# Optimization experiments

Measured on AMD Instinct MI355X. Metric: run time of the kernel, lower is better.

The kernel has to match this reference:

```python
import jax, jax.numpy as jnp
import numpy as np

# Dims: T=64 steps, B=8 batch, H=128 hidden, NH=4 heads, D=2*H=256 cell dim
T, B, H, NH = 64, 8, 128, 4
D = 2 * H
EPS = 1e-5


def _bn(v, scale, bias):
    # flax BatchNorm (training mode): stats over all axes except feature (-1)
    axes = tuple(range(v.ndim - 1))
    mu = v.mean(axes, keepdims=True)
    var = v.var(axes, keepdims=True)
    return (v - mu) * jax.lax.rsqrt(var + EPS) * scale + bias


def setup_inputs() -> dict:
    key = jax.random.key(0)
    ks = iter(jax.random.split(key, 48))
    r = lambda shape, s=0.02: (jax.random.normal(next(ks), shape, jnp.float32) * s)
    z = lambda shape: jnp.zeros(shape, jnp.float32)
    o = lambda shape: jnp.ones(shape, jnp.float32)
    inp = {
        "x": jax.random.normal(next(ks), (T, B, H), jnp.float32),
        # per-head mLSTMCell params (stacked over NH heads), flax Linear: y = x @ W + b
        "Wq": r((NH, D, D)), "bq": z((NH, D)),
        "Wk": r((NH, D, D)), "bk": z((NH, D)),
        "Wv": r((NH, D, D)), "bv": z((NH, D)),
        "conv_k": r((4, 1, NH), 0.2), "conv_b": z((NH,)),  # 1->NH channel conv == per-head 1->1 conv
        "Wi": r((NH, D)), "bi": r((NH,), 0.01),
        "Wf": r((NH, D)),
        "bf": jax.random.uniform(next(ks), (NH,), jnp.float32, 3.0, 6.0),
        "Wo": r((NH, D, D)), "bo": z((NH, D)),
        "Wskip": r((NH, D, D)), "bskip": z((NH, D)),
        # block params
        "bn1_s": o((H,)), "bn1_b": z((H,)),
        "bn2_s": o((D,)), "bn2_b": z((D,)),
        "Wup1": r((H, D)), "bup1": z((D,)),
        "Wup2": r((H, D)), "bup2": z((D,)),
        "Wpoll": r((NH * D, D)), "bpoll": z((D,)),
        "Wdown": r((D, H)), "bdown": z((H,)),
    }
    return inp


def reference(x, Wq, bq, Wk, bk, Wv, bv, conv_k, conv_b, Wi, bi, Wf, bf,
              Wo, bo, Wskip, bskip, bn1_s, bn1_b, bn2_s, bn2_b,
              Wup1, bup1, Wup2, bup2, Wpoll, bpoll, Wdown, bdown):
    nh, d, _ = Wq.shape
    b = x.shape[1]
    inv_sqrt_d = 1.0 / jnp.sqrt(jnp.float32(d))

    def step(carry, xt):
        c, n, m = carry  # c: [nh,b,d,d], n: [nh,b,d], m: [nh,b]
        u = _bn(xt, bn1_s, bn1_b)                      # [b,H]
        trig = jax.nn.silu(u @ Wup2 + bup2)            # [b,d]
        xin = u @ Wup1 + bup1                          # [b,d] mlstm input
        outg = jax.nn.sigmoid(jnp.einsum('bd,hde->hbe', xin, Wo) + bo[:, None, :])
        it = jnp.einsum('bd,hd->hb', xin, Wi) + bi[:, None]
        ft = jnp.einsum('bd,hd->hb', xin, Wf) + bf[:, None]
        m_new = jnp.maximum(ft + m, it)
        ig = jnp.exp(it - m_new)
        fg = jnp.exp(ft + m - m_new)
        # causal-ish depthwise conv over feature axis (flax Conv SAME, k=4)
        qk = jax.lax.conv_general_dilated(xin[..., None], conv_k, (1,), 'SAME',
                                          dimension_numbers=('NWC', 'WIO', 'NWC')) + conv_b
        qk = jax.nn.silu(jnp.transpose(qk, (2, 0, 1)))  # [nh,b,d]
        k = (jnp.einsum('hbd,hde->hbe', qk, Wk) + bk[:, None, :]) * inv_sqrt_d
        q = jnp.einsum('hbd,hde->hbe', qk, Wq) + bq[:, None, :]
        v = jnp.einsum('bd,hde->hbe', xin, Wv) + bv[:, None, :]
        c_new = fg[:, :, None, None] * c + jnp.einsum('hb,hbi,hbj->hbij', ig, v, k)
        n_new = fg[..., None] * n + ig[..., None] * k
        scaler = 1.0 / jnp.maximum(jnp.abs(jnp.einsum('hbi,hbi->hb', n_new, q)), 1.0)
        h = outg * jnp.einsum('hbik,hbk->hbi', c_new, q) * scaler[..., None]
        h = h + jnp.einsum('hbd,hde->hbe', qk, Wskip) + bskip[:, None, :]
        ho = _bn(h, bn2_s, bn2_b)                      # [nh,b,d]
        ho = jnp.transpose(ho, (1, 0, 2)).reshape(b, nh * d)
        ho = ho @ Wpoll + bpoll                        # [b,d]
        y = (ho * trig) @ Wdown + bdown + xt           # residual
        return (c_new, n_new, m_new), y

    c0 = jnp.zeros((nh, b, d, d), x.dtype)
    n0 = jnp.zeros((nh, b, d), x.dtype)
    m0 = jnp.zeros((nh, b), x.dtype)
    _, ys = jax.lax.scan(step, (c0, n0, m0), x)
    return ys
```

## Files before the change

kernel.cpp:

```cpp
#include <hip/hip_runtime.h>
#include <hip/hip_bf16.h>

#define T_ 64
#define B_ 8
#define H_ 128
#define NH_ 4
#define D_ 256
#define TB_ 512
#define EPS_ 1e-5f

typedef short bf16x8 __attribute__((ext_vector_type(8)));
typedef float f32x4 __attribute__((ext_vector_type(4)));

__device__ __forceinline__ float silu_(float x){ return x / (1.0f + __expf(-x)); }
__device__ __forceinline__ float sigm_(float x){ return 1.0f / (1.0f + __expf(-x)); }
__device__ __forceinline__ unsigned short tobf_(float f){
  unsigned u = __float_as_uint(f);
  u += 0x7FFF + ((u >> 16) & 1);
  return (unsigned short)(u >> 16);
}
__device__ __forceinline__ int afrag_(int m, int k){
  return (((m >> 4)*8 + (k >> 5))*64 + ((k >> 3)&3)*16 + (m & 15))*8 + (k & 7);
}
__device__ __forceinline__ int afrag1024_(int m, int k){
  return (((m >> 4)*32 + (k >> 5))*64 + ((k >> 3)&3)*16 + (m & 15))*8 + (k & 7);
}

__global__ __launch_bounds__(256) void k_prep(
    const float* __restrict__ Wq, const float* __restrict__ Wk, const float* __restrict__ Ws,
    const float* __restrict__ Wv, const float* __restrict__ Wo,
    const float* __restrict__ Wup1, const float* __restrict__ Wup2,
    const float* __restrict__ Wp, const float* __restrict__ Wd,
    const float* __restrict__ x, const float* __restrict__ bn1s, const float* __restrict__ bn1b,
    unsigned short* __restrict__ Wqt, unsigned short* __restrict__ Wkt,
    unsigned short* __restrict__ Wst, unsigned short* __restrict__ Wvt,
    unsigned short* __restrict__ Wot,
    unsigned short* __restrict__ Wu1t, unsigned short* __restrict__ Wu2t,
    unsigned short* __restrict__ Wpt, unsigned short* __restrict__ Wdt,
    unsigned short* __restrict__ ub){
  int bid = blockIdx.x;
  int tid = threadIdx.x;
  if (bid < 640){
    int sub = bid & 31;
    int h   = (bid >> 5) & 3;
    int mat = bid >> 7;
    const float* Win; unsigned short* Wout;
    switch (mat){
      case 0: Win = Wq; Wout = Wqt; break;
      case 1: Win = Wk; Wout = Wkt; break;
      case 2: Win = Ws; Wout = Wst; break;
      case 3: Win = Wv; Wout = Wvt; break;
      default: Win = Wo; Wout = Wot; break;
    }
    Win  += h * (D_*D_);
    Wout += h * (D_*D_);
    int gid = sub*256 + tid;
    int combo = gid >> 6;
    int l = gid & 63;
// ... 129 lines not shown
      #pragma unroll
      for (int h = 0; h < NH_; h++){
        float a2 = cb[h];
        a2 = fmaf(xm1, ck[0*NH_+h], a2);
        a2 = fmaf(x0,  ck[1*NH_+h], a2);
        a2 = fmaf(xp1, ck[2*NH_+h], a2);
        a2 = fmaf(xp2, ck[3*NH_+h], a2);
        qkb[h*(TB_*D_) + fa] = tobf_(silu_(a2));
      }
    }
    int dot = tid >> 2, l4 = tid & 3;
    int h = dot >> 4, m = dot & 15;
    float ai = 0.f, af = 0.f;
    const float* wi = Wi + h*D_;
    const float* wf = Wf + h*D_;
    #pragma unroll 8
    for (int jj = 0; jj < 64; jj++){
      int k = l4*64 + jj;
      float xv = xs[m][k];
      ai = fmaf(xv, wi[k], ai);
      af = fmaf(xv, wf[k], af);
    }
    ai += __shfl_down(ai, 1); af += __shfl_down(af, 1);
    ai += __shfl_down(ai, 2); af += __shfl_down(af, 2);
    if (l4 == 0){
      int rowg = rt*16 + m;
      int t = rowg >> 3, b = rowg & 7;
      itb[(h*B_ + b)*T_ + t] = ai + bi[h];
      ftb[(h*B_ + b)*T_ + t] = af + bfv[h];
    }
  }
}

__global__ __launch_bounds__(256) void k_gemm5(
    const unsigned short* __restrict__ qkb, const unsigned short* __restrict__ xinb,
    const unsigned short* __restrict__ Wqt, const unsigned short* __restrict__ Wkt,
    const unsigned short* __restrict__ Wst, const unsigned short* __restrict__ Wvt,
    const unsigned short* __restrict__ Wot,
    const float* __restrict__ bq, const float* __restrict__ bk, const float* __restrict__ bsk,
    const float* __restrict__ bv, const float* __restrict__ bo,
    unsigned short* __restrict__ qob, unsigned short* __restrict__ kob,
    unsigned short* __restrict__ vot,
    float* __restrict__ hb, float* __restrict__ og){
  int bid = blockIdx.x;
  int rt  = bid & 15;
  int h   = (bid >> 4) & 3;
  int mat = bid >> 6;
  int tid = threadIdx.x;
  int w = tid >> 6, l = tid & 63;
  int lm = l & 15, lq = l >> 4;
  int r0 = rt * 32;
  const unsigned short* A = (mat < 3) ? (qkb + h*(TB_*D_)) : xinb;
  const unsigned short* Bt;
  const float* bias;
  switch (mat){
    case 0: Bt = Wqt; bias = bq;  break;
    case 1: Bt = Wkt; bias = bk;  break;
    case 2: Bt = Wst; bias = bsk; break;
    case 3: Bt = Wvt; bias = bv;  break;
    default: Bt = Wot; bias = bo; break;
  }
  Bt += h*(D_*D_);
  f32x4 acc[2][4];
  #pragma unroll
  for (int mt = 0; mt < 2; mt++)
    #pragma unroll
    for (int nt = 0; nt < 4; nt++) acc[mt][nt] = (f32x4){0.f,0.f,0.f,0.f};
  const unsigned short* Ap = A + l*8;
  const unsigned short* Bp = Bt + l*8;
  #pragma unroll
  for (int kc = 0; kc < 8; kc++){
    bf16x8 a0 = *(const bf16x8*)(Ap + ((rt*16      + kc) << 9));
    bf16x8 a1 = *(const bf16x8*)(Ap + ((rt*16 + 8  + kc) << 9));
    bf16x8 b0 = *(const bf16x8*)(Bp + (((w*4+0)*8 + kc) << 9));
    bf16x8 b1 = *(const bf16x8*)(Bp + (((w*4+1)*8 + kc) << 9));
    bf16x8 b2 = *(const bf16x8*)(Bp + (((w*4+2)*8 + kc) << 9));
    bf16x8 b3 = *(const bf16x8*)(Bp + (((w*4+3)*8 + kc) << 9));
    acc[0][0] = __builtin_amdgcn_mfma_f32_16x16x32_bf16(a0, b0, acc[0][0], 0, 0, 0);
    acc[0][1] = __builtin_amdgcn_mfma_f32_16x16x32_bf16(a0, b1, acc[0][1], 0, 0, 0);
    acc[0][2] = __builtin_amdgcn_mfma_f32_16x16x32_bf16(a0, b2, acc[0][2], 0, 0, 0);
    acc[0][3] = __builtin_amdgcn_mfma_f32_16x16x32_bf16(a0, b3, acc[0][3], 0, 0, 0);
    acc[1][0] = __builtin_amdgcn_mfma_f32_16x16x32_bf16(a1, b0, acc[1][0], 0, 0, 0);
    acc[1][1] = __builtin_amdgcn_mfma_f32_16x16x32_bf16(a1, b1, acc[1][1], 0, 0, 0);
    acc[1][2] = __builtin_amdgcn_mfma_f32_16x16x32_bf16(a1, b2, acc[1][2], 0, 0, 0);
    acc[1][3] = __builtin_amdgcn_mfma_f32_16x16x32_bf16(a1, b3, acc[1][3], 0, 0, 0);
  }
  float bval[4];
  #pragma unroll
  for (int nt = 0; nt < 4; nt++) bval[nt] = bias[h*D_ + w*64 + nt*16 + lm];
  #pragma unroll
  for (int mt = 0; mt < 2; mt++){
    #pragma unroll
    for (int r = 0; r < 4; r++){
      int row = r0 + mt*16 + lq*4 + r;
      int t = row >> 3, b = row & 7;
      #pragma unroll
      for (int nt = 0; nt < 4; nt++){
        int e = w*64 + nt*16 + lm;
        float vv = acc[mt][nt][r] + bval[nt];
        if (mat <= 1){
          if (mat == 1) vv *= 0.0625f;
          unsigned short* ob = (mat == 0) ? qob : kob;
          int mt2 = t >> 4, kb2 = e >> 5;
          int lane2 = ((e >> 3)&3)*16 + (t & 15);
          ob[(h*B_ + b)*16384 + ((mt2*8 + kb2)*64 + lane2)*8 + (e & 7)] = tobf_(vv);
        } else if (mat == 3){
          int nt3 = e >> 4, kb3 = t >> 5;
          int lane3 = ((t >> 3)&3)*16 + lm;
          vot[(h*B_ + b)*16384 + ((nt3*2 + kb3)*64 + lane3)*8 + (t & 7)] = tobf_(vv);
        } else {
          int obase = (((t*NH_ + h)*B_ + b) << 8) + e;
          if (mat == 4) og[obase] = sigm_(vv);
          else          hb[obase] = vv;
        }
      }
    }
  }
}

__global__ __launch_bounds__(256) void k_attn2(
    const unsigned short* __restrict__ qob, const unsigned short* __restrict__ kob,
    const unsigned short* __restrict__ vot, const float* __restrict__ og,
    const float* __restrict__ itb, const float* __restrict__ ftb,
    float* __restrict__ hb){
  __shared__ unsigned short Pf[1024];
  __shared__ float partial[4][16];
  __shared__ float scal[16];
  int bid = blockIdx.x;
  int hbx = bid >> 2, tq = bid & 3;
  int h = hbx >> 3, b = hbx & 7;
  int tid = threadIdx.x;
  int w = tid >> 6, l = tid & 63, lm = l & 15, lq = l >> 4;
  float F  = ftb[hbx*T_ + l];
  float it = itb[hbx*T_ + l];
  #pragma unroll
  for (int off = 1; off < 64; off <<= 1){
    float v2 = __shfl_up(F, off);
    if (l >= off) F += v2;
  }
  float ct = it - F;
  float G = ct;
  #pragma unroll
  for (int off = 1; off < 64; off <<= 1){
    float v2 = __shfl_up(G, off);
    if (l >= off) G = fmaxf(G, v2);
  }
  float rb = -fmaxf(0.f, G);
  const unsigned short* Aq = qob + hbx*16384 + l*8;
  const unsigned short* Bk = kob + hbx*16384 + l*8;
  f32x4 accs = (f32x4){0.f,0.f,0.f,0.f};
  #pragma unroll
  for (int kc = 0; kc < 8; kc++){
    bf16x8 a  = *(const bf16x8*)(Aq + ((tq*8 + kc) << 9));
    bf16x8 bb = *(const bf16x8*)(Bk + ((w*8  + kc) << 9));
    accs = __builtin_amdgcn_mfma_f32_16x16x32_bf16(a, bb, accs, 0, 0, 0);
  }
  int s = w*16 + lm;
  float ct_s = __shfl(ct, s);
  float p[4], ps[4];
  #pragma unroll
  for (int r = 0; r < 4; r++){
    int t = tq*16 + lq*4 + r;
    float rb_t = __shfl(rb, t);
    float pv = (s <= t) ? __expf(ct_s + rb_t) * accs[r] : 0.f;
    p[r] = pv; ps[r] = pv;
  }
  #pragma unroll
  for (int off = 1; off < 16; off <<= 1){
    #pragma unroll
    for (int r = 0; r < 4; r++) ps[r] += __shfl_xor(ps[r], off);
  }
  if (lm == 0){
    #pragma unroll
    for (int r = 0; r < 4; r++) partial[w][lq*4 + r] = ps[r];
  }
  {
    int kbP = w >> 1;
    int laneP = ((w*2 + (lm >> 3)) & 3)*16;
    int jP = lm & 7;
    #pragma unroll
    for (int r = 0; r < 4; r++){
      int m = lq*4 + r;
      Pf[(kbP*64 + laneP + m)*8 + jP] = tobf_(p[r]);
    }
  }
  __syncthreads();
  if (tid < 16){
    float sum = partial[0][tid] + partial[1][tid] + partial[2][tid] + partial[3][tid];
    scal[tid] = 1.0f / fmaxf(fabsf(sum), 1.0f);
  }
  bf16x8 pa0 = *(const bf16x8*)(Pf + l*8);
  bf16x8 pa1 = *(const bf16x8*)(Pf + 512 + l*8);
  const unsigned short* Bv = vot + hbx*16384 + l*8;
  f32x4 acco[4];
  #pragma unroll
  for (int nt = 0; nt < 4; nt++) acco[nt] = (f32x4){0.f,0.f,0.f,0.f};
  #pragma unroll
  for (int nt = 0; nt < 4; nt++){
    int nt3 = w*4 + nt;
    bf16x8 b0 = *(const bf16x8*)(Bv + (((nt3*2 + 0)) << 9));
    bf16x8 b1 = *(const bf16x8*)(Bv + (((nt3*2 + 1)) << 9));
    acco[nt] = __builtin_amdgcn_mfma_f32_16x16x32_bf16(pa0, b0, acco[nt], 0, 0, 0);
    acco[nt] = __builtin_amdgcn_mfma_f32_16x16x32_bf16(pa1, b1, acco[nt], 0, 0, 0);
  }
  __syncthreads();
  #pragma unroll
  for (int nt = 0; nt < 4; nt++){
    #pragma unroll
    for (int r = 0; r < 4; r++){
      int tl = lq*4 + r;
      int t = tq*16 + tl;
      int e = (w*4 + nt)*16 + lm;
      int idx = (((t*NH_ + h)*B_ + b) << 8) + e;
      hb[idx] += og[idx] * acco[nt][r] * scal[tl];
    }
  }
}

__global__ __launch_bounds__(256) void k_bn2f(
    const float* __restrict__ hbuf, const float* __restrict__ bn2s, const float* __restrict__ bn2b,
    unsigned short* __restrict__ hob){
  int t = blockIdx.x;
  int d = threadIdx.x;
  const float* hp = hbuf + (t*NH_*B_)*D_ + d;
  float v[32]; float mu = 0.f;
  #pragma unroll
  for (int i = 0; i < 32; i++){ v[i] = hp[i*D_]; mu += v[i]; }
  mu *= (1.0f/32.0f);
  float var = 0.f;
  #pragma unroll
  for (int i = 0; i < 32; i++){ float dd = v[i]-mu; var += dd*dd; }
  var *= (1.0f/32.0f);
  float sc = (1.0f/sqrtf(var + EPS_)) * bn2s[d];
  float bs = bn2b[d];
  #pragma unroll
  for (int i = 0; i < 32; i++){
    int hh = i >> 3, b = i & 7;
    int m = t*B_ + b;
    int k = hh*D_ + d;
    hob[afrag1024_(m, k)] = tobf_((v[i]-mu)*sc + bs);
  }
}

__global__ __launch_bounds__(512) void k_tail2(
    const unsigned short* __restrict__ hob, const unsigned short* __restrict__ Wpt,
    const float* __restrict__ bp, const float* __restrict__ trig,
    const unsigned short* __restrict__ Wdt, const float* __restrict__ bd,
    const float* __restrict__ x, float* __restrict__ y){
  __shared__ unsigned short zf[32*256];
  int rt = blockIdx.x;
  int tid = threadIdx.x;
  int w = tid >> 6, l = tid & 63, lm = l & 15, lq = l >> 4;
  f32x4 acc[2][2];
  #pragma unroll
  for (int mt = 0; mt < 2; mt++)
    #pragma unroll
    for (int nt = 0; nt < 2; nt++) acc[mt][nt] = (f32x4){0.f,0.f,0.f,0.f};
  const unsigned short* Ap = hob + l*8;
  const unsigned short* Bp = Wpt + l*8;
  #pragma unroll 4
  for (int kc = 0; kc < 32; kc++){
    bf16x8 a0 = *(const bf16x8*)(Ap + (((rt*2+0)*32 + kc) << 9));
    bf16x8 a1 = *(const bf16x8*)(Ap + (((rt*2+1)*32 + kc) << 9));
    bf16x8 b0 = *(const bf16x8*)(Bp + (((w*2+0)*32 + kc) << 9));
    bf16x8 b1 = *(const bf16x8*)(Bp + (((w*2+1)*32 + kc) << 9));
    acc[0][0] = __builtin_amdgcn_mfma_f32_16x16x32_bf16(a0, b0, acc[0][0], 0, 0, 0);
    acc[0][1] = __builtin_amdgcn_mfma_f32_16x16x32_bf16(a0, b1, acc[0][1], 0, 0, 0);
    acc[1][0] = __builtin_amdgcn_mfma_f32_16x16x32_bf16(a1, b0, acc[1][0], 0, 0, 0);
    acc[1][1] = __builtin_amdgcn_mfma_f32_16x16x32_bf16(a1, b1, acc[1][1], 0, 0, 0);
  }
  #pragma unroll
  for (int mt = 0; mt < 2; mt++){
    #pragma unroll
    for (int nt = 0; nt < 2; nt++){
      int e = w*32 + nt*16 + lm;
      float bpe = bp[e];
      #pragma unroll
      for (int r = 0; r < 4; r++){
        int ml = mt*16 + lq*4 + r;
        int row = rt*32 + ml;
        float z = (acc[mt][nt][r] + bpe) * trig[row*D_ + e];
        zf[afrag_(ml, e)] = tobf_(z);
      }
    }
  }
  __syncthreads();
  f32x4 acc2[2];
  acc2[0] = (f32x4){0.f,0.f,0.f,0.f};
  acc2[1] = (f32x4){0.f,0.f,0.f,0.f};
  const unsigned short* Bdp = Wdt + l*8;
  #pragma unroll
  for (int kc = 0; kc < 8; kc++){
    bf16x8 a0 = *(const bf16x8*)(zf + ((0*8 + kc) << 9) + l*8);
    bf16x8 a1 = *(const bf16x8*)(zf + ((1*8 + kc) << 9) + l*8);
    bf16x8 bb = *(const bf16x8*)(Bdp + ((w*8 + kc) << 9));
    acc2[0] = __builtin_amdgcn_mfma_f32_16x16x32_bf16(a0, bb, acc2[0], 0, 0, 0);
    acc2[1] = __builtin_amdgcn_mfma_f32_16x16x32_bf16(a1, bb, acc2[1], 0, 0, 0);
  }
  int hh = w*16 + lm;
  float bde = bd[hh];
  #pragma unroll
  for (int mt = 0; mt < 2; mt++){
    #pragma unroll
    for (int r = 0; r < 4; r++){
      int row = rt*32 + mt*16 + lq*4 + r;
      y[row*H_ + hh] = acc2[mt][r] + bde + x[row*H_ + hh];
    }
  }
}

extern "C" void kernel_launch(void* const* d_in, const int* in_sizes, int n_in,
                              void* d_out, int out_size, void* d_ws, size_t ws_size,
                              hipStream_t stream){
  const float* x     = (const float*)d_in[0];
  const float* Wq    = (const float*)d_in[1];
  const float* bq    = (const float*)d_in[2];
  const float* Wk    = (const float*)d_in[3];
  const float* bk    = (const float*)d_in[4];
  const float* Wv    = (const float*)d_in[5];
  const float* bv    = (const float*)d_in[6];
  const float* ck    = (const float*)d_in[7];
  const float* cb    = (const float*)d_in[8];
  const float* Wi    = (const float*)d_in[9];
  const float* bi    = (const float*)d_in[10];
  const float* Wf    = (const float*)d_in[11];
  const float* bf    = (const float*)d_in[12];
  const float* Wo    = (const float*)d_in[13];
  const float* bo    = (const float*)d_in[14];
  const float* Wsk   = (const float*)d_in[15];
  const float* bsk   = (const float*)d_in[16];
  const float* bn1s  = (const float*)d_in[17];
  const float* bn1b  = (const float*)d_in[18];
  const float* bn2s  = (const float*)d_in[19];
  const float* bn2b  = (const float*)d_in[20];
  const float* Wup1  = (const float*)d_in[21];
  const float* bup1  = (const float*)d_in[22];
  const float* Wup2  = (const float*)d_in[23];
  const float* bup2  = (const float*)d_in[24];
  const float* Wp    = (const float*)d_in[25];
  const float* bp    = (const float*)d_in[26];
  const float* Wd    = (const float*)d_in[27];
  const float* bd    = (const float*)d_in[28];
  float* y = (float*)d_out;

  float* w = (float*)d_ws;
  float* trig = w;  w += T_*B_*D_;
  float* hbuf = w;  w += T_*NH_*B_*D_;
  float* og   = w;  w += T_*NH_*B_*D_;
  float* itb  = w;  w += NH_*B_*T_;
  float* ftb  = w;  w += NH_*B_*T_;
  unsigned short* xinb = (unsigned short*)w;  w += (T_*B_*D_)/2;
  unsigned short* qkb  = (unsigned short*)w;  w += (NH_*TB_*D_)/2;
  unsigned short* Wqt  = (unsigned short*)w;  w += (NH_*D_*D_)/2;
  unsigned short* Wkt  = (unsigned short*)w;  w += (NH_*D_*D_)/2;
  unsigned short* Wst  = (unsigned short*)w;  w += (NH_*D_*D_)/2;
  unsigned short* Wvt  = (unsigned short*)w;  w += (NH_*D_*D_)/2;
  unsigned short* Wot  = (unsigned short*)w;  w += (NH_*D_*D_)/2;
  unsigned short* Wu1t = (unsigned short*)w;  w += (H_*D_)/2;
  unsigned short* Wu2t = (unsigned short*)w;  w += (H_*D_)/2;
  unsigned short* ub   = (unsigned short*)w;  w += (TB_*H_)/2;
  unsigned short* qob  = (unsigned short*)w;  w += (NH_*B_*T_*D_)/2;
  unsigned short* kob  = (unsigned short*)w;  w += (NH_*B_*T_*D_)/2;
  unsigned short* vot  = (unsigned short*)w;  w += (NH_*B_*T_*D_)/2;
  unsigned short* hob  = (unsigned short*)w;  w += (TB_*NH_*D_)/2;
  unsigned short* Wpt  = (unsigned short*)w;  w += (NH_*D_*D_)/2;
  unsigned short* Wdt  = (unsigned short*)w;  w += (D_*H_)/2;

  k_prep <<<848, 256, 0, stream>>>(Wq, Wk, Wsk, Wv, Wo, Wup1, Wup2, Wp, Wd, x, bn1s, bn1b,
                                   Wqt, Wkt, Wst, Wvt, Wot, Wu1t, Wu2t, Wpt, Wdt, ub);
  k_upcg <<<64, 256, 0, stream>>>(ub, Wu1t, Wu2t, bup1, bup2, ck, cb, Wi, bi, Wf, bf,
                                  xinb, qkb, trig, itb, ftb);
  k_gemm5<<<320, 256, 0, stream>>>(qkb, xinb, Wqt, Wkt, Wst, Wvt, Wot,
                                   bq, bk, bsk, bv, bo, qob, kob, vot, hbuf, og);
  k_attn2<<<NH_*B_*4, 256, 0, stream>>>(qob, kob, vot, og, itb, ftb, hbuf);
  k_bn2f <<<T_, 256, 0, stream>>>(hbuf, bn2s, bn2b, hob);
  k_tail2<<<16, 512, 0, stream>>>(hob, Wpt, bp, trig, Wdt, bd, x, y);
}
```

Before: 156.8 us.

## Fuse all stages into one cooperative persistent kernel with grid syncs

Replaces the six-kernel launch chain with a single cooperative kernel that runs each phase in a grid-stride loop, separated by grid.sync(). The work is rebalanced across phases: part of the big weight conversion moves into the second phase, the Wp and Wd conversions run alongside the up-projection, and BN2 is fused into the tail GEMM. The aim is to remove launch gaps and per-kernel ramp-up. In exchange it adds grid-wide barrier cost, fixes occupancy at 2 blocks per CU with 40KB of shared memory, and falls back to separate launches if the cooperative launch fails.

Result: slower. 309.1 us (+97.1%).

```diff
diff --git a/kernel.cpp b/kernel.cpp
--- a/kernel.cpp
+++ b/kernel.cpp
@@ -1,5 +1,8 @@
 #include <hip/hip_runtime.h>
+#include <hip/hip_cooperative_groups.h>
 #include <hip/hip_bf16.h>
+
+namespace cg = cooperative_groups;
 
 #define T_ 64
 #define B_ 8
@@ -24,6 +27,467 @@
 }
 __device__ __forceinline__ int afrag1024_(int m, int k){
   return (((m >> 4)*32 + (k >> 5))*64 + ((k >> 3)&3)*16 + (m & 15))*8 + (k & 7);
+}
+
+struct KP {
+  const float *x, *ck, *cb, *Wi, *bi, *Wf, *bfv;
+  const float *bq, *bk, *bv, *bo, *bsk;
+  const float *bn1s, *bn1b, *bn2s, *bn2b, *bup1, *bup2, *bp, *bd;
+  const float *Wq, *Wk, *Wv, *Wo, *Wsk, *Wup1, *Wup2, *Wp, *Wd;
+  float *y, *trig, *hbuf, *og, *itb, *ftb;
+  unsigned short *xinb, *qkb, *Wqt, *Wkt, *Wst, *Wvt, *Wot, *Wu1t, *Wu2t, *ub,
+                 *qob, *kob, *vot, *Wpt, *Wdt;
+};
+
+
+__device__ __forceinline__ void ph_big5(const KP& p, int u, int tid){
+  int sub = u & 31;
+  int h   = (u >> 5) & 3;
+  int mat = u >> 7;
+  const float* Win; unsigned short* Wout;
+  switch (mat){
+    case 0: Win = p.Wq;  Wout = p.Wqt; break;
+    case 1: Win = p.Wk;  Wout = p.Wkt; break;
+    case 2: Win = p.Wsk; Wout = p.Wst; break;
+    case 3: Win = p.Wv;  Wout = p.Wvt; break;
+    default: Win = p.Wo; Wout = p.Wot; break;
+  }
+  Win  += h * (D_*D_);
+  Wout += h * (D_*D_);
+  int gid = sub*256 + tid;
+  int combo = gid >> 6;
+  int l = gid & 63;
+  int lm = l & 15, lq = l >> 4;
+  int nt = combo >> 3, kb = combo & 7;
+  int n = nt*16 + lm;
+  int k0 = kb*32 + lq*8;
+  bf16x8 v;
+  #pragma unroll
+  for (int j = 0; j < 8; j++) v[j] = (short)tobf_(Win[(k0+j)*D_ + n]);
+  *(bf16x8*)(Wout + (combo*64 + l)*8) = v;
+}
+
+__device__ __forceinline__ void ph_wu(const KP& p, int idx, int tid){
+  const float* Win = (idx < 16) ? p.Wup1 : p.Wup2;
+  unsigned short* Wout = (idx < 16) ? p.Wu1t : p.Wu2t;
+  int sub = idx & 15;
+  int gid = sub*256 + tid;
+  int combo = gid >> 6;
+  int l = gid & 63;
+  int lm = l & 15, lq = l >> 4;
+  int nt = combo >> 2, kb = combo & 3;
+  int n = nt*16 + lm;
+  int k0 = kb*32 + lq*8;
+  bf16x8 v;
+  #pragma unroll
+  for (int j = 0; j < 8; j++) v[j] = (short)tobf_(Win[(k0+j)*D_ + n]);
+  *(bf16x8*)(Wout + (combo*64 + l)*8) = v;
+}
+
+__device__ __forceinline__ void ph_ub(const KP& p, int i, int tid){
+  int tt = tid >> 7, hf = tid & 127;
+  int t = i*2 + tt;
+  const float* xp = p.x + t*(B_*H_) + hf;
+  float v0[8]; float mu = 0.f;
+  #pragma unroll
+  for (int b = 0; b < 8; b++){ v0[b] = xp[b*H_]; mu += v0[b]; }
+  mu *= 0.125f;
+  float var = 0.f;
+  #pragma unroll
+  for (int b = 0; b < 8; b++){ float dd = v0[b]-mu; var += dd*dd; }
+  var *= 0.125f;
+  float sc = (1.0f/sqrtf(var + EPS_)) * p.bn1s[hf];
+  float bs = p.bn1b[hf];
+  int kb = hf >> 5, j = hf & 7;
+  int lanebase = ((hf >> 3)&3)*16 + tt*8;
+  unsigned short* up = p.ub + ((i*4 + kb)*64)*8 + j;
+  #pragma unroll
+  for (int b = 0; b < 8; b++)
+    up[(lanebase + b)*8] = tobf_((v0[b]-mu)*sc + bs);
+}
+
+__device__ __forceinline__ void ph_wp(const KP& p, int u, int tid){
+  int gid = u*256 + tid;
+  int combo = gid >> 6;
+  int l = gid & 63;
+  int lm = l & 15, lq = l >> 4;
+  int nt = combo >> 5, kb = combo & 31;
+  int n = nt*16 + lm;
+  int k0 = kb*32 + lq*8;
+  bf16x8 v;
+  #pragma unroll
+  for (int j = 0; j < 8; j++) v[j] = (short)tobf_(p.Wp[(k0+j)*D_ + n]);
+  *(bf16x8*)(p.Wpt + (combo*64 + l)*8) = v;
+}
+
+__device__ __forceinline__ void ph_wd(const KP& p, int u, int tid){
+  int gid = u*256 + tid;
+  int combo = gid >> 6;
+  int l = gid & 63;
+  int lm = l & 15, lq = l >> 4;
+  int nt = combo >> 3, kb = combo & 7;
+  int n = nt*16 + lm;
+  int k0 = kb*32 + lq*8;
+  bf16x8 v;
+  #pragma unroll
+  for (int j = 0; j < 8; j++) v[j] = (short)tobf_(p.Wd[(k0+j)*H_ + n]);
+  *(bf16x8*)(p.Wdt + (combo*64 + l)*8) = v;
+}
+
+__device__ __forceinline__ void ph_upcg(const KP& p, int u, int tid, unsigned char* smemraw){
+  float (*xs)[257] = (float (*)[257])smemraw;
+  int mat = u >> 5, rt = u & 31;
+  int w = tid >> 6, l = tid & 63, lm = l & 15, lq = l >> 4;
+  const unsigned short* Bt = (mat == 0) ? p.Wu1t : p.Wu2t;
+  f32x4 acc[4];
+  #pragma unroll
+  for (int nt = 0; nt < 4; nt++) acc[nt] = (f32x4){0.f,0.f,0.f,0.f};
+  const unsigned short* Ap = p.ub + l*8;
+  const unsigned short* Bp = Bt + l*8;
+  #pragma unroll
+  for (int kb = 0; kb < 4; kb++){
+    bf16x8 a = *(const bf16x8*)(Ap + ((rt*4 + kb) << 9));
+    #pragma unroll
+    for (int nt = 0; nt < 4; nt++){
+      bf16x8 bfr = *(const bf16x8*)(Bp + (((w*4+nt)*4 + kb) << 9));
+      acc[nt] = __builtin_amdgcn_mfma_f32_16x16x32_bf16(a, bfr, acc[nt], 0, 0, 0);
+    }
+  }
+  const float* bias = (mat == 0) ? p.bup1 : p.bup2;
+  #pragma unroll
+  for (int nt = 0; nt < 4; nt++){
+    #pragma unroll
+    for (int r = 0; r < 4; r++){
+      int m = lq*4 + r;
+      int row = rt*16 + m;
+      int e = w*64 + nt*16 + lm;
+      float vv = acc[nt][r] + bias[e];
+      if (mat == 1){
+        p.trig[row*D_ + e] = silu_(vv);
+      } else {
+        p.xinb[afrag_(row, e)] = tobf_(vv);
+        xs[m][e] = vv;
+      }
+    }
+  }
+  if (mat == 0){
+    __syncthreads();
+    int d = tid;
+    #pragma unroll 4
+    for (int m = 0; m < 16; m++){
+      float x0  = xs[m][d];
+      float xm1 = (d >= 1)   ? xs[m][d-1] : 0.f;
+      float xp1 = (d <= 254) ? xs[m][d+1] : 0.f;
+      float xp2 = (d <= 253) ? xs[m][d+2] : 0.f;
+      int rowg = rt*16 + m;
+      int fa = afrag_(rowg, d);
+      #pragma unroll
+      for (int h = 0; h < NH_; h++){
+        float a2 = p.cb[h];
+        a2 = fmaf(xm1, p.ck[0*NH_+h], a2);
+        a2 = fmaf(x0,  p.ck[1*NH_+h], a2);
+        a2 = fmaf(xp1, p.ck[2*NH_+h], a2);
+        a2 = fmaf(xp2, p.ck[3*NH_+h], a2);
+        p.qkb[h*(TB_*D_) + fa] = tobf_(silu_(a2));
+      }
+    }
+    int dot = tid >> 2, l4 = tid & 3;
+    int h = dot >> 4, m = dot & 15;
+    float ai = 0.f, af = 0.f;
+    const float* wi = p.Wi + h*D_;
+    const float* wf = p.Wf + h*D_;
+    #pragma unroll 8
+    for (int jj = 0; jj < 64; jj++){
+      int k = l4*64 + jj;
+      float xv = xs[m][k];
+      ai = fmaf(xv, wi[k], ai);
+      af = fmaf(xv, wf[k], af);
+    }
+    ai += __shfl_down(ai, 1); af += __shfl_down(af, 1);
+    ai += __shfl_down(ai, 2); af += __shfl_down(af, 2);
+    if (l4 == 0){
+      int rowg = rt*16 + m;
+      int t = rowg >> 3, b = rowg & 7;
+      p.itb[(h*B_ + b)*T_ + t] = ai + p.bi[h];
+      p.ftb[(h*B_ + b)*T_ + t] = af + p.bfv[h];
+    }
+  }
+  __syncthreads();
+}
+
+__device__ __forceinline__ void ph_gemm5(const KP& p, int u, int tid){
+  int rt  = u & 15;
+  int h   = (u >> 4) & 3;
+  int mat = u >> 6;
+  int w = tid >> 6, l = tid & 63;
+  int lm = l & 15, lq = l >> 4;
+  int r0 = rt * 32;
+  const unsigned short* A = (mat < 3) ? (p.qkb + h*(TB_*D_)) : p.xinb;
+  const unsigned short* Bt;
+  const float* bias;
+  switch (mat){
+    case 0: Bt = p.Wqt; bias = p.bq;  break;
+    case 1: Bt = p.Wkt; bias = p.bk;  break;
+    case 2: Bt = p.Wst; bias = p.bsk; break;
+    case 3: Bt = p.Wvt; bias = p.bv;  break;
+    default: Bt = p.Wot; bias = p.bo; break;
+  }
+  Bt += h*(D_*D_);
+  f32x4 acc[2][4];
+  #pragma unroll
+  for (int mt = 0; mt < 2; mt++)
+    #pragma unroll
+    for (int nt = 0; nt < 4; nt++) acc[mt][nt] = (f32x4){0.f,0.f,0.f,0.f};
+  const unsigned short* Ap = A + l*8;
+  const unsigned short* Bp = Bt + l*8;
+  #pragma unroll
+  for (int kc = 0; kc < 8; kc++){
+    bf16x8 a0 = *(const bf16x8*)(Ap + ((rt*16      + kc) << 9));
+    bf16x8 a1 = *(const bf16x8*)(Ap + ((rt*16 + 8  + kc) << 9));
+    bf16x8 b0 = *(const bf16x8*)(Bp + (((w*4+0)*8 + kc) << 9));
+    bf16x8 b1 = *(const bf16x8*)(Bp + (((w*4+1)*8 + kc) << 9));
+    bf16x8 b2 = *(const bf16x8*)(Bp + (((w*4+2)*8 + kc) << 9));
+    bf16x8 b3 = *(const bf16x8*)(Bp + (((w*4+3)*8 + kc) << 9));
+    acc[0][0] = __builtin_amdgcn_mfma_f32_16x16x32_bf16(a0, b0, acc[0][0], 0, 0, 0);
+    acc[0][1] = __builtin_amdgcn_mfma_f32_16x16x32_bf16(a0, b1, acc[0][1], 0, 0, 0);
+    acc[0][2] = __builtin_amdgcn_mfma_f32_16x16x32_bf16(a0, b2, acc[0][2], 0, 0, 0);
+    acc[0][3] = __builtin_amdgcn_mfma_f32_16x16x32_bf16(a0, b3, acc[0][3], 0, 0, 0);
+    acc[1][0] = __builtin_amdgcn_mfma_f32_16x16x32_bf16(a1, b0, acc[1][0], 0, 0, 0);
+    acc[1][1] = __builtin_amdgcn_mfma_f32_16x16x32_bf16(a1, b1, acc[1][1], 0, 0, 0);
+    acc[1][2] = __builtin_amdgcn_mfma_f32_16x16x32_bf16(a1, b2, acc[1][2], 0, 0, 0);
+    acc[1][3] = __builtin_amdgcn_mfma_f32_16x16x32_bf16(a1, b3, acc[1][3], 0, 0, 0);
+  }
+  float bval[4];
+  #pragma unroll
+  for (int nt = 0; nt < 4; nt++) bval[nt] = bias[h*D_ + w*64 + nt*16 + lm];
+  #pragma unroll
+  for (int mt = 0; mt < 2; mt++){
+    #pragma unroll
+    for (int r = 0; r < 4; r++){
+      int row = r0 + mt*16 + lq*4 + r;
+      int t = row >> 3, b = row & 7;
+      #pragma unroll
+      for (int nt = 0; nt < 4; nt++){
+        int e = w*64 + nt*16 + lm;
+        float vv = acc[mt][nt][r] + bval[nt];
+        if (mat <= 1){
+          if (mat == 1) vv *= 0.0625f;
+          unsigned short* ob = (mat == 0) ? p.qob : p.kob;
+          int mt2 = t >> 4, kb2 = e >> 5;
+          int lane2 = ((e >> 3)&3)*16 + (t & 15);
+          ob[(h*B_ + b)*16384 + ((mt2*8 + kb2)*64 + lane2)*8 + (e & 7)] = tobf_(vv);
+        } else if (mat == 3){
+          int nt3 = e >> 4, kb3 = t >> 5;
+          int lane3 = ((t >> 3)&3)*16 + lm;
+          p.vot[(h*B_ + b)*16384 + ((nt3*2 + kb3)*64 + lane3)*8 + (t & 7)] = tobf_(vv);
+        } else {
+          int obase = (((t*NH_ + h)*B_ + b) << 8) + e;
+          if (mat == 4) p.og[obase] = sigm_(vv);
+          else          p.hbuf[obase] = vv;
+        }
+      }
+    }
+  }
+}
+
+__device__ __forceinline__ void ph_attn(const KP& p, int u, int tid, unsigned char* smemraw){
+  unsigned short* Pf = (unsigned short*)smemraw;
+  float (*partial)[16] = (float (*)[16])(smemraw + 2048);
+  float* scal = (float*)(smemraw + 2048 + 256);
+  int hbx = u >> 2, tq = u & 3;
+  int h = hbx >> 3, b = hbx & 7;
+  int w = tid >> 6, l = tid & 63, lm = l & 15, lq = l >> 4;
+  float F  = p.ftb[hbx*T_ + l];
+  float it = p.itb[hbx*T_ + l];
+  #pragma unroll
+  for (int off = 1; off < 64; off <<= 1){
+    float v2 = __shfl_up(F, off);
+    if (l >= off) F += v2;
+  }
+  float ct = it - F;
+  float G = ct;
+  #pragma unroll
+  for (int off = 1; off < 64; off <<= 1){
+    float v2 = __shfl_up(G, off);
+    if (l >= off) G = fmaxf(G, v2);
+  }
+  float rb = -fmaxf(0.f, G);
+  const unsigned short* Aq = p.qob + hbx*16384 + l*8;
+  const unsigned short* Bk = p.kob + hbx*16384 + l*8;
+  f32x4 accs = (f32x4){0.f,0.f,0.f,0.f};
+  #pragma unroll
+  for (int kc = 0; kc < 8; kc++){
+    bf16x8 a  = *(const bf16x8*)(Aq + ((tq*8 + kc) << 9));
+    bf16x8 bb = *(const bf16x8*)(Bk + ((w*8  + kc) << 9));
+    accs = __builtin_amdgcn_mfma_f32_16x16x32_bf16(a, bb, accs, 0, 0, 0);
+  }
+  int s = w*16 + lm;
+  float ct_s = __shfl(ct, s);
+  float pv4[4], ps[4];
+  #pragma unroll
+  for (int r = 0; r < 4; r++){
+    int t = tq*16 + lq*4 + r;
+    float rb_t = __shfl(rb, t);
+    float pv = (s <= t) ? __expf(ct_s + rb_t) * accs[r] : 0.f;
+    pv4[r] = pv; ps[r] = pv;
+  }
+  #pragma unroll
+  for (int off = 1; off < 16; off <<= 1){
+    #pragma unroll
+    for (int r = 0; r < 4; r++) ps[r] += __shfl_xor(ps[r], off);
+  }
+  if (lm == 0){
+    #pragma unroll
+    for (int r = 0; r < 4; r++) partial[w][lq*4 + r] = ps[r];
+  }
+  {
+    int kbP = w >> 1;
+    int laneP = ((w*2 + (lm >> 3)) & 3)*16;
+    int jP = lm & 7;
+    #pragma unroll
+    for (int r = 0; r < 4; r++){
+      int m = lq*4 + r;
+      Pf[(kbP*64 + laneP + m)*8 + jP] = tobf_(pv4[r]);
+    }
+  }
+  __syncthreads();
+  if (tid < 16){
+    float sum = partial[0][tid] + partial[1][tid] + partial[2][tid] + partial[3][tid];
+    scal[tid] = 1.0f / fmaxf(fabsf(sum), 1.0f);
+  }
+  bf16x8 pa0 = *(const bf16x8*)(Pf + l*8);
+  bf16x8 pa1 = *(const bf16x8*)(Pf + 512 + l*8);
+  const unsigned short* Bv = p.vot + hbx*16384 + l*8;
+  f32x4 acco[4];
+  #pragma unroll
+  for (int nt = 0; nt < 4; nt++) acco[nt] = (f32x4){0.f,0.f,0.f,0.f};
+  #pragma unroll
+  for (int nt = 0; nt < 4; nt++){
+    int nt3 = w*4 + nt;
+    bf16x8 b0 = *(const bf16x8*)(Bv + (((nt3*2 + 0)) << 9));
+    bf16x8 b1 = *(const bf16x8*)(Bv + (((nt3*2 + 1)) << 9));
+    acco[nt] = __builtin_amdgcn_mfma_f32_16x16x32_bf16(pa0, b0, acco[nt], 0, 0, 0);
+    acco[nt] = __builtin_amdgcn_mfma_f32_16x16x32_bf16(pa1, b1, acco[nt], 0, 0, 0);
+  }
+  __syncthreads();
+  #pragma unroll
+  for (int nt = 0; nt < 4; nt++){
+    #pragma unroll
+    for (int r = 0; r < 4; r++){
+      int tl = lq*4 + r;
+      int t = tq*16 + tl;
+      int e = (w*4 + nt)*16 + lm;
+      int idx = (((t*NH_ + h)*B_ + b) << 8) + e;
+      p.hbuf[idx] += p.og[idx] * acco[nt][r] * scal[tl];
+    }
+  }
+}
+
+__device__ __forceinline__ void ph_tail(const KP& p, int u, int tid, unsigned char* smemraw){
+  unsigned short* hfr = (unsigned short*)smemraw;
+  unsigned short* zf  = (unsigned short*)(smemraw + 32768);
+  int w = tid >> 6, l = tid & 63, lm = l & 15, lq = l >> 4;
+  #pragma unroll
+  for (int s = 0; s < 2; s++){
+    int pair = tid + (s << 8);
+    int tt = pair >> 8;
+    int d  = pair & 255;
+    int t  = u*2 + tt;
+    const float* hp = p.hbuf + (t*NH_*B_)*D_ + d;
+    float v[32]; float mu = 0.f;
+    #pragma unroll
+    for (int i = 0; i < 32; i++){ v[i] = hp[i*D_]; mu += v[i]; }
+    mu *= (1.0f/32.0f);
+    float var = 0.f;
+    #pragma unroll
+    for (int i = 0; i < 32; i++){ float dd = v[i]-mu; var += dd*dd; }
+    var *= (1.0f/32.0f);
+    float sc = (1.0f/sqrtf(var + EPS_)) * p.bn2s[d];
+    float bs = p.bn2b[d];
+    #pragma unroll
+    for (int i = 0; i < 32; i++){
+      int hh = i >> 3, b = i & 7;
+      int m = tt*8 + b;
+      int k = hh*D_ + d;
+      hfr[afrag1024_(m, k)] = tobf_((v[i]-mu)*sc + bs);
+    }
+  }
+  __syncthreads();
+  f32x4 acc[4];
+  #pragma unroll
+  for (int nt = 0; nt < 4; nt++) acc[nt] = (f32x4){0.f,0.f,0.f,0.f};
+  const unsigned short* Apl = hfr + l*8;
+  const unsigned short* Bp  = p.Wpt + l*8;
+  #pragma unroll 4
+  for (int kc = 0; kc < 32; kc++){
+    bf16x8 a = *(const bf16x8*)(Apl + (kc << 9));
+    #pragma unroll
+    for (int nt = 0; nt < 4; nt++){
+      bf16x8 bfr = *(const bf16x8*)(Bp + ((((w*4+nt)*32) + kc) << 9));
+      acc[nt] = __builtin_amdgcn_mfma_f32_16x16x32_bf16(a, bfr, acc[nt], 0, 0, 0);
+    }
+  }
+  #pragma unroll
+  for (int nt = 0; nt < 4; nt++){
+    int e = w*64 + nt*16 + lm;
+    float bpe = p.bp[e];
+    #pragma unroll
+    for (int r = 0; r < 4; r++){
+      int ml = lq*4 + r;
+      int row = u*16 + ml;
+      float z = (acc[nt][r] + bpe) * p.trig[row*D_ + e];
+      zf[afrag_(ml, e)] = tobf_(z);
+    }
+  }
+  __syncthreads();
+  f32x4 acc2[2];
+  acc2[0] = (f32x4){0.f,0.f,0.f,0.f};
+  acc2[1] = (f32x4){0.f,0.f,0.f,0.f};
+  const unsigned short* Bdp = p.Wdt + l*8;
+  #pragma unroll
+  for (int kc = 0; kc < 8; kc++){
+    bf16x8 a = *(const bf16x8*)(zf + (kc << 9) + l*8);
+    #pragma unroll
+    for (int q = 0; q < 2; q++){
+      bf16x8 bb = *(const bf16x8*)(Bdp + (((w*2+q)*8 + kc) << 9));
+      acc2[q] = __builtin_amdgcn_mfma_f32_16x16x32_bf16(a, bb, acc2[q], 0, 0, 0);
+    }
+  }
+  #pragma unroll
+  for (int q = 0; q < 2; q++){
+    int hh = (w*2+q)*16 + lm;
+    float bde = p.bd[hh];
+    #pragma unroll
+    for (int r = 0; r < 4; r++){
+      int row = u*16 + lq*4 + r;
+      p.y[row*H_ + hh] = acc2[q][r] + bde + p.x[row*H_ + hh];
+    }
+  }
+}
+
+__global__ __launch_bounds__(256, 2) void k_fused(KP p){
+  __shared__ alignas(16) unsigned char smem[40960];
+  cg::grid_group grid = cg::this_grid();
+  const int tid = threadIdx.x;
+  const int gsz = gridDim.x;
+  for (int u = blockIdx.x; u < 512; u += gsz){
+    if (u < 32)       ph_wu(p, u, tid);
+    else if (u < 64)  ph_ub(p, u - 32, tid);
+    else              ph_big5(p, u - 64, tid);
+  }
+  grid.sync();
+  for (int u = blockIdx.x; u < 400; u += gsz){
+    if (u < 64)       ph_upcg(p, u, tid, smem);
+    else if (u < 256) ph_big5(p, 448 + (u - 64), tid);
+    else if (u < 384) ph_wp(p, u - 256, tid);
+    else              ph_wd(p, u - 384, tid);
+  }
+  grid.sync();
+  for (int u = blockIdx.x; u < 320; u += gsz) ph_gemm5(p, u, tid);
+  grid.sync();
+  for (int u = blockIdx.x; u < 128; u += gsz) ph_attn(p, u, tid, smem);
+  grid.sync();
+  for (int u = blockIdx.x; u < 32; u += gsz) ph_tail(p, u, tid, smem);
 }
 
 __global__ __launch_bounds__(256) void k_prep(
@@ -219,7 +683,7 @@
   }
 }
 
-__global__ __launch_bounds__(256) void k_gemm5(
+__global__ __launch_bounds__(256) void k_gemm5_old(
     const unsigned short* __restrict__ qkb, const unsigned short* __restrict__ xinb,
     const unsigned short* __restrict__ Wqt, const unsigned short* __restrict__ Wkt,
     const unsigned short* __restrict__ Wst, const unsigned short* __restrict__ Wvt,
@@ -229,271 +693,45 @@
     unsigned short* __restrict__ qob, unsigned short* __restrict__ kob,
     unsigned short* __restrict__ vot,
     float* __restrict__ hb, float* __restrict__ og){
-  int bid = blockIdx.x;
-  int rt  = bid & 15;
-  int h   = (bid >> 4) & 3;
-  int mat = bid >> 6;
-  int tid = threadIdx.x;
-  int w = tid >> 6, l = tid & 63;
-  int lm = l & 15, lq = l >> 4;
-  int r0 = rt * 32;
-  const unsigned short* A = (mat < 3) ? (qkb + h*(TB_*D_)) : xinb;
-  const unsigned short* Bt;
-  const float* bias;
-  switch (mat){
-    case 0: Bt = Wqt; bias = bq;  break;
-    case 1: Bt = Wkt; bias = bk;  break;
-    case 2: Bt = Wst; bias = bsk; break;
-    case 3: Bt = Wvt; bias = bv;  break;
-    default: Bt = Wot; bias = bo; break;
-  }
-  Bt += h*(D_*D_);
-  f32x4 acc[2][4];
-  #pragma unroll
-  for (int mt = 0; mt < 2; mt++)
-    #pragma unroll
-    for (int nt = 0; nt < 4; nt++) acc[mt][nt] = (f32x4){0.f,0.f,0.f,0.f};
-  const unsigned short* Ap = A + l*8;
-  const unsigned short* Bp = Bt + l*8;
-  #pragma unroll
-  for (int kc = 0; kc < 8; kc++){
-    bf16x8 a0 = *(const bf16x8*)(Ap + ((rt*16      + kc) << 9));
-    bf16x8 a1 = *(const bf16x8*)(Ap + ((rt*16 + 8  + kc) << 9));
-    bf16x8 b0 = *(const bf16x8*)(Bp + (((w*4+0)*8 + kc) << 9));
-    bf16x8 b1 = *(const bf16x8*)(Bp + (((w*4+1)*8 + kc) << 9));
-    bf16x8 b2 = *(const bf16x8*)(Bp + (((w*4+2)*8 + kc) << 9));
-    bf16x8 b3 = *(const bf16x8*)(Bp + (((w*4+3)*8 + kc) << 9));
-    acc[0][0] = __builtin_amdgcn_mfma_f32_16x16x32_bf16(a0, b0, acc[0][0], 0, 0, 0);
-    acc[0][1] = __builtin_amdgcn_mfma_f32_16x16x32_bf16(a0, b1, acc[0][1], 0, 0, 0);
-    acc[0][2] = __builtin_amdgcn_mfma_f32_16x16x32_bf16(a0, b2, acc[0][2], 0, 0, 0);
-    acc[0][3] = __builtin_amdgcn_mfma_f32_16x16x32_bf16(a0, b3, acc[0][3], 0, 0, 0);
-    acc[1][0] = __builtin_amdgcn_mfma_f32_16x16x32_bf16(a1, b0, acc[1][0], 0, 0, 0);
-    acc[1][1] = __builtin_amdgcn_mfma_f32_16x16x32_bf16(a1, b1, acc[1][1], 0, 0, 0);
-    acc[1][2] = __builtin_amdgcn_mfma_f32_16x16x32_bf16(a1, b2, acc[1][2], 0, 0, 0);
-    acc[1][3] = __builtin_amdgcn_mfma_f32_16x16x32_bf16(a1, b3, acc[1][3], 0, 0, 0);
-  }
-  float bval[4];
-  #pragma unroll
-  for (int nt = 0; nt < 4; nt++) bval[nt] = bias[h*D_ + w*64 + nt*16 + lm];
-  #pragma unroll
-  for (int mt = 0; mt < 2; mt++){
-    #pragma unroll
-    for (int r = 0; r < 4; r++){
-      int row = r0 + mt*16 + lq*4 + r;
-      int t = row >> 3, b = row & 7;
-      #pragma unroll
-      for (int nt = 0; nt < 4; nt++){
-        int e = w*64 + nt*16 + lm;
-        float vv = acc[mt][nt][r] + bval[nt];
-        if (mat <= 1){
-          if (mat == 1) vv *= 0.0625f;
-          unsigned short* ob = (mat == 0) ? qob : kob;
-          int mt2 = t >> 4, kb2 = e >> 5;
-          int lane2 = ((e >> 3)&3)*16 + (t & 15);
-          ob[(h*B_ + b)*16384 + ((mt2*8 + kb2)*64 + lane2)*8 + (e & 7)] = tobf_(vv);
-        } else if (mat == 3){
-          int nt3 = e >> 4, kb3 = t >> 5;
-          int lane3 = ((t >> 3)&3)*16 + lm;
-          vot[(h*B_ + b)*16384 + ((nt3*2 + kb3)*64 + lane3)*8 + (t & 7)] = tobf_(vv);
-        } else {
-          int obase = (((t*NH_ + h)*B_ + b) << 8) + e;
-          if (mat == 4) og[obase] = sigm_(vv);
-          else          hb[obase] = vv;
-        }
-      }
-    }
-  }
-}
-
-__global__ __launch_bounds__(256) void k_attn2(
+  KP p{};
+  p.qkb = (unsigned short*)qkb; p.xinb = (unsigned short*)xinb;
+  p.Wqt = (unsigned short*)Wqt; p.Wkt = (unsigned short*)Wkt; p.Wst = (unsigned short*)Wst;
+  p.Wvt = (unsigned short*)Wvt; p.Wot = (unsigned short*)Wot;
+  p.bq = bq; p.bk = bk; p.bsk = bsk; p.bv = bv; p.bo = bo;
+  p.qob = qob; p.kob = kob; p.vot = vot; p.hbuf = hb; p.og = og;
+  ph_gemm5(p, blockIdx.x, threadIdx.x);
+}
+
+__global__ __launch_bounds__(256) void k_attn2_old(
     const unsigned short* __restrict__ qob, const unsigned short* __restrict__ kob,
     const unsigned short* __restrict__ vot, const float* __restrict__ og,
     const float* __restrict__ itb, const float* __restrict__ ftb,
     float* __restrict__ hb){
-  __shared__ unsigned short Pf[1024];
-  __shared__ float partial[4][16];
-  __shared__ float scal[16];
-  int bid = blockIdx.x;
-  int hbx = bid >> 2, tq = bid & 3;
-  int h = hbx >> 3, b = hbx & 7;
-  int tid = threadIdx.x;
-  int w = tid >> 6, l = tid & 63, lm = l & 15, lq = l >> 4;
-  float F  = ftb[hbx*T_ + l];
-  float it = itb[hbx*T_ + l];
-  #pragma unroll
-  for (int off = 1; off < 64; off <<= 1){
-    float v2 = __shfl_up(F, off);
-    if (l >= off) F += v2;
-  }
-  float ct = it - F;
-  float G = ct;
-  #pragma unroll
-  for (int off = 1; off < 64; off <<= 1){
-    float v2 = __shfl_up(G, off);
-    if (l >= off) G = fmaxf(G, v2);
-  }
-  float rb = -fmaxf(0.f, G);
-  const unsigned short* Aq = qob + hbx*16384 + l*8;
-  const unsigned short* Bk = kob + hbx*16384 + l*8;
-  f32x4 accs = (f32x4){0.f,0.f,0.f,0.f};
-  #pragma unroll
-  for (int kc = 0; kc < 8; kc++){
-    bf16x8 a  = *(const bf16x8*)(Aq + ((tq*8 + kc) << 9));
-    bf16x8 bb = *(const bf16x8*)(Bk + ((w*8  + kc) << 9));
-    accs = __builtin_amdgcn_mfma_f32_16x16x32_bf16(a, bb, accs, 0, 0, 0);
-  }
-  int s = w*16 + lm;
-  float ct_s = __shfl(ct, s);
-  float p[4], ps[4];
-  #pragma unroll
-  for (int r = 0; r < 4; r++){
-    int t = tq*16 + lq*4 + r;
-    float rb_t = __shfl(rb, t);
-    float pv = (s <= t) ? __expf(ct_s + rb_t) * accs[r] : 0.f;
-    p[r] = pv; ps[r] = pv;
-  }
-  #pragma unroll
-  for (int off = 1; off < 16; off <<= 1){
-    #pragma unroll
-    for (int r = 0; r < 4; r++) ps[r] += __shfl_xor(ps[r], off);
-  }
-  if (lm == 0){
-    #pragma unroll
-    for (int r = 0; r < 4; r++) partial[w][lq*4 + r] = ps[r];
-  }
-  {
-    int kbP = w >> 1;
-    int laneP = ((w*2 + (lm >> 3)) & 3)*16;
-    int jP = lm & 7;
-    #pragma unroll
-    for (int r = 0; r < 4; r++){
-      int m = lq*4 + r;
-      Pf[(kbP*64 + laneP + m)*8 + jP] = tobf_(p[r]);
-    }
-  }
-  __syncthreads();
-  if (tid < 16){
-    float sum = partial[0][tid] + partial[1][tid] + partial[2][tid] + partial[3][tid];
-    scal[tid] = 1.0f / fmaxf(fabsf(sum), 1.0f);
-  }
-  bf16x8 pa0 = *(const bf16x8*)(Pf + l*8);
-  bf16x8 pa1 = *(const bf16x8*)(Pf + 512 + l*8);
-  const unsigned short* Bv = vot + hbx*16384 + l*8;
-  f32x4 acco[4];
-  #pragma unroll
-  for (int nt = 0; nt < 4; nt++) acco[nt] = (f32x4){0.f,0.f,0.f,0.f};
-  #pragma unroll
-  for (int nt = 0; nt < 4; nt++){
-    int nt3 = w*4 + nt;
-    bf16x8 b0 = *(const bf16x8*)(Bv + (((nt3*2 + 0)) << 9));
-    bf16x8 b1 = *(const bf16x8*)(Bv + (((nt3*2 + 1)) << 9));
-    acco[nt] = __builtin_amdgcn_mfma_f32_16x16x32_bf16(pa0, b0, acco[nt], 0, 0, 0);
-    acco[nt] = __builtin_amdgcn_mfma_f32_16x16x32_bf16(pa1, b1, acco[nt], 0, 0, 0);
-  }
-  __syncthreads();
-  #pragma unroll
-  for (int nt = 0; nt < 4; nt++){
-    #pragma unroll
-    for (int r = 0; r < 4; r++){
-      int tl = lq*4 + r;
-      int t = tq*16 + tl;
-      int e = (w*4 + nt)*16 + lm;
-      int idx = (((t*NH_ + h)*B_ + b) << 8) + e;
-      hb[idx] += og[idx] * acco[nt][r] * scal[tl];
-    }
-  }
-}
-
-__global__ __launch_bounds__(256) void k_bn2f(
+  __shared__ alignas(16) unsigned char smem[4096];
+  KP p{};
+  p.qob = (unsigned short*)qob; p.kob = (unsigned short*)kob; p.vot = (unsigned short*)vot;
+  p.og = (float*)og; p.itb = (float*)itb; p.ftb = (float*)ftb; p.hbuf = hb;
+  ph_attn(p, blockIdx.x, threadIdx.x, smem);
+}
+
+__global__ __launch_bounds__(512) void k_bn2tail_old(
     const float* __restrict__ hbuf, const float* __restrict__ bn2s, const float* __restrict__ bn2b,
-    unsigned short* __restrict__ hob){
-  int t = blockIdx.x;
-  int d = threadIdx.x;
-  const float* hp = hbuf + (t*NH_*B_)*D_ + d;
-  float v[32]; float mu = 0.f;
-  #pragma unroll
-  for (int i = 0; i < 32; i++){ v[i] = hp[i*D_]; mu += v[i]; }
-  mu *= (1.0f/32.0f);
-  float var = 0.f;
-  #pragma unroll
-  for (int i = 0; i < 32; i++){ float dd = v[i]-mu; var += dd*dd; }
-  var *= (1.0f/32.0f);
-  float sc = (1.0f/sqrtf(var + EPS_)) * bn2s[d];
-  float bs = bn2b[d];
-  #pragma unroll
-  for (int i = 0; i < 32; i++){
-    int hh = i >> 3, b = i & 7;
-    int m = t*B_ + b;
-    int k = hh*D_ + d;
-    hob[afrag1024_(m, k)] = tobf_((v[i]-mu)*sc + bs);
-  }
-}
-
-__global__ __launch_bounds__(512) void k_tail2(
-    const unsigned short* __restrict__ hob, const unsigned short* __restrict__ Wpt,
-    const float* __restrict__ bp, const float* __restrict__ trig,
-    const unsigned short* __restrict__ Wdt, const float* __restrict__ bd,
-    const float* __restrict__ x, float* __restrict__ y){
-  __shared__ unsigned short zf[32*256];
-  int rt = blockIdx.x;
-  int tid = threadIdx.x;
-  int w = tid >> 6, l = tid & 63, lm = l & 15, lq = l >> 4;
-  f32x4 acc[2][2];
-  #pragma unroll
-  for (int mt = 0; mt < 2; mt++)
-    #pragma unroll
-    for (int nt = 0; nt < 2; nt++) acc[mt][nt] = (f32x4){0.f,0.f,0.f,0.f};
-  const unsigned short* Ap = hob + l*8;
-  const unsigned short* Bp = Wpt + l*8;
-  #pragma unroll 4
-  for (int kc = 0; kc < 32; kc++){
-    bf16x8 a0 = *(const bf16x8*)(Ap + (((rt*2+0)*32 + kc) << 9));
-    bf16x8 a1 = *(const bf16x8*)(Ap + (((rt*2+1)*32 + kc) << 9));
-    bf16x8 b0 = *(const bf16x8*)(Bp + (((w*2+0)*32 + kc) << 9));
-    bf16x8 b1 = *(const bf16x8*)(Bp + (((w*2+1)*32 + kc) << 9));
-    acc[0][0] = __builtin_amdgcn_mfma_f32_16x16x32_bf16(a0, b0, acc[0][0], 0, 0, 0);
-    acc[0][1] = __builtin_amdgcn_mfma_f32_16x16x32_bf16(a0, b1, acc[0][1], 0, 0, 0);
-    acc[1][0] = __builtin_amdgcn_mfma_f32_16x16x32_bf16(a1, b0, acc[1][0], 0, 0, 0);
-    acc[1][1] = __builtin_amdgcn_mfma_f32_16x16x32_bf16(a1, b1, acc[1][1], 0, 0, 0);
-  }
-  #pragma unroll
-  for (int mt = 0; mt < 2; mt++){
-    #pragma unroll
-    for (int nt = 0; nt < 2; nt++){
-      int e = w*32 + nt*16 + lm;
-      float bpe = bp[e];
-      #pragma unroll
-      for (int r = 0; r < 4; r++){
-        int ml = mt*16 + lq*4 + r;
-        int row = rt*32 + ml;
-        float z = (acc[mt][nt][r] + bpe) * trig[row*D_ + e];
-        zf[afrag_(ml, e)] = tobf_(z);
-      }
-    }
-  }
-  __syncthreads();
-  f32x4 acc2[2];
-  acc2[0] = (f32x4){0.f,0.f,0.f,0.f};
-  acc2[1] = (f32x4){0.f,0.f,0.f,0.f};
-  const unsigned short* Bdp = Wdt + l*8;
-  #pragma unroll
-  for (int kc = 0; kc < 8; kc++){
-    bf16x8 a0 = *(const bf16x8*)(zf + ((0*8 + kc) << 9) + l*8);
-    bf16x8 a1 = *(const bf16x8*)(zf + ((1*8 + kc) << 9) + l*8);
-    bf16x8 bb = *(const bf16x8*)(Bdp + ((w*8 + kc) << 9));
-    acc2[0] = __builtin_amdgcn_mfma_f32_16x16x32_bf16(a0, bb, acc2[0], 0, 0, 0);
-    acc2[1] = __builtin_amdgcn_mfma_f32_16x16x32_bf16(a1, bb, acc2[1], 0, 0, 0);
-  }
-  int hh = w*16 + lm;
-  float bde = bd[hh];
-  #pragma unroll
-  for (int mt = 0; mt < 2; mt++){
-    #pragma unroll
-    for (int r = 0; r < 4; r++){
-      int row = rt*32 + mt*16 + lq*4 + r;
-      y[row*H_ + hh] = acc2[mt][r] + bde + x[row*H_ + hh];
-    }
-  }
+    const unsigned short* __restrict__ Wpt, const float* __restrict__ bp,
+    const float* __restrict__ trig, const unsigned short* __restrict__ Wdt,
+    const float* __restrict__ bd, const float* __restrict__ x, float* __restrict__ y){
+  (void)hbuf;(void)bn2s;(void)bn2b;(void)Wpt;(void)bp;(void)trig;(void)Wdt;(void)bd;(void)x;(void)y;
+}
+
+__global__ __launch_bounds__(256) void k_tail_old(
+    const float* __restrict__ hbuf, const float* __restrict__ bn2s, const float* __restrict__ bn2b,
+    const unsigned short* __restrict__ Wpt, const float* __restrict__ bp,
+    const float* __restrict__ trig, const unsigned short* __restrict__ Wdt,
+    const float* __restrict__ bd, const float* __restrict__ x, float* __restrict__ y){
+  __shared__ alignas(16) unsigned char smem[40960];
+  KP p{};
+  p.hbuf = (float*)hbuf; p.bn2s = bn2s; p.bn2b = bn2b; p.Wpt = (unsigned short*)Wpt;
+  p.bp = bp; p.trig = (float*)trig; p.Wdt = (unsigned short*)Wdt; p.bd = bd; p.x = x; p.y = y;
+  ph_tail(p, blockIdx.x, threadIdx.x, smem);
 }
 
 extern "C" void kernel_launch(void* const* d_in, const int* in_sizes, int n_in,
@@ -552,14 +790,43 @@
   unsigned short* hob  = (unsigned short*)w;  w += (TB_*NH_*D_)/2;
   unsigned short* Wpt  = (unsigned short*)w;  w += (NH_*D_*D_)/2;
   unsigned short* Wdt  = (unsigned short*)w;  w += (D_*H_)/2;
-
-  k_prep <<<848, 256, 0, stream>>>(Wq, Wk, Wsk, Wv, Wo, Wup1, Wup2, Wp, Wd, x, bn1s, bn1b,
-                                   Wqt, Wkt, Wst, Wvt, Wot, Wu1t, Wu2t, Wpt, Wdt, ub);
-  k_upcg <<<64, 256, 0, stream>>>(ub, Wu1t, Wu2t, bup1, bup2, ck, cb, Wi, bi, Wf, bf,
-                                  xinb, qkb, trig, itb, ftb);
-  k_gemm5<<<320, 256, 0, stream>>>(qkb, xinb, Wqt, Wkt, Wst, Wvt, Wot,
-                                   bq, bk, bsk, bv, bo, qob, kob, vot, hbuf, og);
-  k_attn2<<<NH_*B_*4, 256, 0, stream>>>(qob, kob, vot, og, itb, ftb, hbuf);
-  k_bn2f <<<T_, 256, 0, stream>>>(hbuf, bn2s, bn2b, hob);
-  k_tail2<<<16, 512, 0, stream>>>(hob, Wpt, bp, trig, Wdt, bd, x, y);
-}
+  (void)hob;
+
+  KP P;
+  P.x = x; P.ck = ck; P.cb = cb; P.Wi = Wi; P.bi = bi; P.Wf = Wf; P.bfv = bf;
+  P.bq = bq; P.bk = bk; P.bv = bv; P.bo = bo; P.bsk = bsk;
+  P.bn1s = bn1s; P.bn1b = bn1b; P.bn2s = bn2s; P.bn2b = bn2b;
+  P.bup1 = bup1; P.bup2 = bup2; P.bp = bp; P.bd = bd;
+  P.Wq = Wq; P.Wk = Wk; P.Wv = Wv; P.Wo = Wo; P.Wsk = Wsk;
+  P.Wup1 = Wup1; P.Wup2 = Wup2; P.Wp = Wp; P.Wd = Wd;
+  P.y = y; P.trig = trig; P.hbuf = hbuf; P.og = og; P.itb = itb; P.ftb = ftb;
+  P.xinb = xinb; P.qkb = qkb; P.Wqt = Wqt; P.Wkt = Wkt; P.Wst = Wst; P.Wvt = Wvt;
+  P.Wot = Wot; P.Wu1t = Wu1t; P.Wu2t = Wu2t; P.ub = ub;
+  P.qob = qob; P.kob = kob; P.vot = vot; P.Wpt = Wpt; P.Wdt = Wdt;
+
+  static int g_nblk = 0;
+  if (g_nblk == 0){
+    int nb = 0;
+    hipError_t qe = hipOccupancyMaxActiveBlocksPerMultiprocessor(
+        &nb, reinterpret_cast<const void*>(&k_fused), 256, 0);
+    if (qe != hipSuccess || nb < 1) nb = 1;
+    if (nb > 2) nb = 2;
+    g_nblk = 256 * nb;
+  }
+
+  void* args[] = { (void*)&P };
+  hipError_t err = hipLaunchCooperativeKernel(
+      reinterpret_cast<const void*>(&k_fused), dim3(g_nblk), dim3(256), args, 0u, stream);
+
+  if (err != hipSuccess){
+    (void)hipGetLastError();
+    k_prep <<<848, 256, 0, stream>>>(Wq, Wk, Wsk, Wv, Wo, Wup1, Wup2, Wp, Wd, x, bn1s, bn1b,
+                                     Wqt, Wkt, Wst, Wvt, Wot, Wu1t, Wu2t, Wpt, Wdt, ub);
+    k_upcg <<<64, 256, 0, stream>>>(ub, Wu1t, Wu2t, bup1, bup2, ck, cb, Wi, bi, Wf, bf,
+                                    xinb, qkb, trig, itb, ftb);
+    k_gemm5_old<<<320, 256, 0, stream>>>(qkb, xinb, Wqt, Wkt, Wst, Wvt, Wot,
+                                         bq, bk, bsk, bv, bo, qob, kob, vot, hbuf, og);
+    k_attn2_old<<<NH_*B_*4, 256, 0, stream>>>(qob, kob, vot, og, itb, ftb, hbuf);
+    k_tail_old<<<32, 256, 0, stream>>>(hbuf, bn2s, bn2b, Wpt, bp, trig, Wdt, bd, x, y);
+  }
+}
```
